# Kernel tuning notes

Measured on AMD Instinct MI355X. Metric: run time of the kernel, lower is better.

## Reference

```python
import jax, jax.numpy as jnp
import numpy as np

N_NODES = 100000
N_EDGES = 3200000
D_IN = 128
D_OUT = 128
LN_EPS = 1e-5


def setup_inputs() -> dict:
    key = jax.random.key(0)
    k1, k2, k3, k4 = jax.random.split(key, 4)
    x = jax.random.normal(k1, (N_NODES, D_IN), dtype=jnp.float32)
    edge_index = jax.random.randint(k2, (2, N_EDGES), 0, N_NODES, dtype=jnp.int64)
    # GCNConv weight (glorot-ish scale) and bias
    W = jax.random.normal(k3, (D_IN, D_OUT), dtype=jnp.float32) / np.sqrt(D_IN)
    b = jnp.zeros((D_OUT,), dtype=jnp.float32)
    # LayerNorm params
    gamma = jnp.ones((D_OUT,), dtype=jnp.float32)
    beta = jnp.zeros((D_OUT,), dtype=jnp.float32)
    return {"x": x, "edge_index": edge_index, "W": W, "b": b, "gamma": gamma, "beta": beta}


def reference(x, edge_index, W, b, gamma, beta):
    # GCNConv: add self-loops, symmetric degree normalization, aggregate, add bias.
    N = x.shape[0]
    self_loops = jnp.arange(N, dtype=edge_index.dtype)
    row = jnp.concatenate([edge_index[0], self_loops])  # destination
    col = jnp.concatenate([edge_index[1], self_loops])  # source
    deg = jax.ops.segment_sum(jnp.ones(row.shape[0], x.dtype), row, num_segments=N)
    dinv = jnp.where(deg > 0, jax.lax.rsqrt(deg), 0.0)
    norm = dinv[row] * dinv[col]                         # [E+N]
    xw = x @ W                                           # [N, D_OUT]
    msg = norm[:, None] * xw[col]                        # gather + scale [E+N, D_OUT]
    agg = jax.ops.segment_sum(msg, row, num_segments=N) + b  # scatter-add
    # LayerNorm over feature dim
    mu = jnp.mean(agg, axis=-1, keepdims=True)
    var = jnp.mean(jnp.square(agg - mu), axis=-1, keepdims=True)
    h = (agg - mu) * jax.lax.rsqrt(var + LN_EPS) * gamma + beta
    # ReLU; Dropout is identity in eval mode
    return jax.nn.relu(h)
```

## Files before the change

### kernel.cpp

```cpp
#include <hip/hip_runtime.h>

#define N_NODES 100000
#define N_EDGES 3200000
#define D 128
#define NB 782
#define BCAP 5120
#define STAGE 16
#define NKEY 1024

typedef __attribute__((ext_vector_type(8))) short bf16x8;
typedef __attribute__((ext_vector_type(4))) float f32x4;

__device__ __forceinline__ float bf2f(unsigned short u) {
  return __uint_as_float(((unsigned)u) << 16);
}
__device__ __forceinline__ unsigned short f2bf(float f) {
  unsigned u = __float_as_uint(f);
  u += 0x7FFF + ((u >> 16) & 1);
  return (unsigned short)(u >> 16);
}

__global__ void detect_kernel(const int* __restrict__ ei32, int* __restrict__ flag) {
  __shared__ int anynz;
  if (threadIdx.x == 0) anynz = 0;
  __syncthreads();
  int v = 0;
  for (int i = threadIdx.x; i < 2048; i += 256) v |= ei32[2 * i + 1];
  if (v) atomicOr(&anynz, 1);
  __syncthreads();
  if (threadIdx.x == 0) *flag = (anynz == 0) ? 1 : 0;
}

__global__ void prep_w_kernel(const float* __restrict__ W, unsigned short* __restrict__ wTg) {
  int t = threadIdx.x;
  int c = t >> 1, h = t & 1;
  for (int k0 = h * 64; k0 < h * 64 + 64; k0 += 8) {
    unsigned short tmp[8];
#pragma unroll
    for (int j = 0; j < 8; j++) tmp[j] = f2bf(W[(k0 + j) * D + c]);
    *(uint4*)(wTg + c * D + k0) = *(uint4*)tmp;
  }
}

__global__ __launch_bounds__(256) void partition_kernel(const void* __restrict__ edges,
                                                        const int* __restrict__ flag,
                                                        int* __restrict__ gcur,
                                                        unsigned int* __restrict__ bstore) {
  __shared__ unsigned int stage[NB][STAGE];
  __shared__ int scnt[NB];
  const bool is64 = (*flag != 0);
  for (int i = threadIdx.x; i < NB; i += 256) scnt[i] = 0;
  __syncthreads();
  int gstride = gridDim.x * blockDim.x;
  for (int base = blockIdx.x * blockDim.x; base < N_EDGES; base += gstride) {
    int e = base + threadIdx.x;
    if (e < N_EDGES) {
      int r, c;
      if (is64) {
        r = (int)((const long long*)edges)[e];
        c = (int)((const long long*)edges)[N_EDGES + e];
      } else {
        r = ((const int*)edges)[e];
        c = ((const int*)edges)[N_EDGES + e];
      }
      int b = r >> 7;
      unsigned ent = ((unsigned)(r & 127) << 17) | (unsigned)c;
      int pos = atomicAdd(&scnt[b], 1);
      if (pos < STAGE) {
        stage[b][pos] = ent;
      } else {
        int gp = atomicAdd(&gcur[b], 1);
        if (gp < BCAP) bstore[(size_t)b * BCAP + gp] = ent;
      }
    }
    __syncthreads();
    for (int b = threadIdx.x; b < NB; b += 256) {
      if (scnt[b] >= STAGE) {
        int gp = atomicAdd(&gcur[b], STAGE);
        if (gp + STAGE <= BCAP) {
          uint4* dst = (uint4*)&bstore[(size_t)b * BCAP + gp];
          uint4* src = (uint4*)&stage[b][0];
          dst[0] = src[0];
          dst[1] = src[1];
          dst[2] = src[2];
          dst[3] = src[3];
        } else {
          for (int k = 0; k < STAGE; k++)
            if (gp + k < BCAP) bstore[(size_t)b * BCAP + gp + k] = stage[b][k];
        }
        scnt[b] = 0;
      }
    }
    __syncthreads();
  }
  for (int b = threadIdx.x; b < NB; b += 256) {
    int n = scnt[b];
    if (n > STAGE) n = STAGE;
    if (n > 0) {
      int gp = atomicAdd(&gcur[b], n);
      for (int k = 0; k < n; k++)
        if (gp + k < BCAP) bstore[(size_t)b * BCAP + gp + k] = stage[b][k];
    }
  }
}

__global__ __launch_bounds__(256) void bucket_kernel(const int* __restrict__ gcur,
                                                     unsigned int* __restrict__ bstore,
                                                     int* __restrict__ cnt,
                                                     int* __restrict__ start,
                                                     float* __restrict__ dinv) {
  __shared__ unsigned int ent[BCAP];
  __shared__ int kc[NKEY];
  __shared__ int koff[NKEY];
  __shared__ int psum[256];
  int b = blockIdx.x, tid = threadIdx.x;
  size_t base = (size_t)b * BCAP;
  int m = gcur[b];
  if (m > BCAP) m = BCAP;
  int nodes = N_NODES - b * 128;
  if (nodes > 128) nodes = 128;

  for (int i = tid; i < m; i += 256) ent[i] = bstore[base + i];
  for (int i = tid; i < NKEY; i += 256) kc[i] = 0;
  __syncthreads();
  for (int i = tid; i < m; i += 256) {
    unsigned u = ent[i];
    int key = (int)(((u >> 17) << 3) | ((u & 0x1FFFFu) >> 14));
    atomicAdd(&kc[key], 1);
  }
  __syncthreads();
  int c0 = kc[4 * tid], c1 = kc[4 * tid + 1], c2 = kc[4 * tid + 2], c3 = kc[4 * tid + 3];
  psum[tid] = c0 + c1 + c2 + c3;
  __syncthreads();
#pragma unroll
  for (int off = 1; off < 256; off <<= 1) {
    int v = (tid >= off) ? psum[tid - off] : 0;
    __syncthreads();
    psum[tid] += v;
    __syncthreads();
  }
  int o = (tid == 0) ? 0 : psum[tid - 1];
  kc[4 * tid] = o;
  kc[4 * tid + 1] = o + c0;
  kc[4 * tid + 2] = o + c0 + c1;
  kc[4 * tid + 3] = o + c0 + c1 + c2;
  koff[4 * tid] = o;
  koff[4 * tid + 1] = o + c0;
  koff[4 * tid + 2] = o + c0 + c1;
  koff[4 * tid + 3] = o + c0 + c1 + c2;
  __syncthreads();
  if (tid < nodes) {
    int st = kc[8 * tid];
    int en = (tid == 127) ? m : kc[8 * (tid + 1)];
    int node = b * 128 + tid;
    start[node] = (int)base + st;
    cnt[node] = en - st;
    dinv[node] = rsqrtf((float)(en - st + 1));
  }
  __syncthreads();
  for (int i = tid; i < m; i += 256) {
    unsigned u = ent[i];
    int key = (int)(((u >> 17) << 3) | ((u & 0x1FFFFu) >> 14));
    int pos = atomicAdd(&koff[key], 1);
    bstore[base + pos] = u & 0x1FFFF;
  }
}

__global__ __launch_bounds__(256) void gemm_mfma_kernel(const float* __restrict__ x,
                                                        const unsigned short* __restrict__ wTg,
                                                        const float* __restrict__ dinv,
                                                        unsigned short* __restrict__ y) {
  __shared__ unsigned short xs[64 * 136];
  __shared__ unsigned short wls[128 * 136];
  int tid = threadIdx.x;
  int row0 = blockIdx.x * 64;
  {
    int c = tid >> 1, h = tid & 1;
    const uint4* src = (const uint4*)(wTg + c * D + h * 64);
    uint4* dst = (uint4*)(wls + c * 136 + h * 64);
#pragma unroll
    for (int i = 0; i < 8; i++) dst[i] = src[i];
  }
  {
    int rx = tid >> 2, q = tid & 3;
    int r = row0 + rx;
    if (r > N_NODES - 1) r = N_NODES - 1;
    const float4* src = (const float4*)(x + (size_t)r * D + q * 32);
    uint4* dst = (uint4*)(xs + rx * 136 + q * 32);
#pragma unroll
    for (int i = 0; i < 4; i++) {
      float4 fa = src[2 * i], fb = src[2 * i + 1];
      uint4 p;
      p.x = (unsigned)f2bf(fa.x) | ((unsigned)f2bf(fa.y) << 16);
      p.y = (unsigned)f2bf(fa.z) | ((unsigned)f2bf(fa.w) << 16);
      p.z = (unsigned)f2bf(fb.x) | ((unsigned)f2bf(fb.y) << 16);
      p.w = (unsigned)f2bf(fb.z) | ((unsigned)f2bf(fb.w) << 16);
      dst[i] = p;
    }
  }
  __syncthreads();
  int w = tid >> 6, l = tid & 63;
  int g = l >> 4, ln = l & 15;
  bf16x8 af[4];
#pragma unroll
  for (int kt = 0; kt < 4; kt++)
    af[kt] = *(const bf16x8*)(xs + (w * 16 + ln) * 136 + kt * 32 + g * 8);
  int rbase = row0 + w * 16 + 4 * g;
  float dv[4];
#pragma unroll
  for (int j = 0; j < 4; j++) {
    int r = rbase + j;
    dv[j] = dinv[r < N_NODES ? r : N_NODES - 1];
  }
#pragma unroll
  for (int ct = 0; ct < 8; ct++) {
    f32x4 acc = {0.f, 0.f, 0.f, 0.f};
#pragma unroll
    for (int kt = 0; kt < 4; kt++) {
      bf16x8 bf = *(const bf16x8*)(wls + (ct * 16 + ln) * 136 + kt * 32 + g * 8);
      acc = __builtin_amdgcn_mfma_f32_16x16x32_bf16(af[kt], bf, acc, 0, 0, 0);
    }
#pragma unroll
    for (int j = 0; j < 4; j++) {
      int r = rbase + j;
      if (r < N_NODES) y[(size_t)r * D + ct * 16 + ln] = f2bf(dv[j] * acc[j]);
    }
  }
}

__global__ __launch_bounds__(256) void agg_ln_kernel(
    const unsigned short* __restrict__ y, const unsigned int* __restrict__ csr,
    const int* __restrict__ start, const int* __restrict__ cnt,
    const float* __restrict__ dinv, const float* __restrict__ bias,
    const float* __restrict__ gamma, const float* __restrict__ beta,
    float* __restrict__ out) {
  int wid = threadIdx.x >> 6, lane = threadIdx.x & 63;
  int node = blockIdx.x * 4 + wid;
  if (node >= N_NODES) return;
  int q = lane >> 4, hl = lane & 15;
  int s = start[node];
  int n = cnt[node];
  float a0 = 0.f, a1 = 0.f, a2 = 0.f, a3 = 0.f, a4 = 0.f, a5 = 0.f, a6 = 0.f, a7 = 0.f;
  const unsigned short* yq = y + hl * 8;
#define ACC(V)                                       \
  a0 += __uint_as_float((V).x << 16);                \
  a1 += __uint_as_float((V).x & 0xFFFF0000u);        \
  a2 += __uint_as_float((V).y << 16);                \
  a3 += __uint_as_float((V).y & 0xFFFF0000u);        \
  a4 += __uint_as_float((V).z << 16);                \
  a5 += __uint_as_float((V).z & 0xFFFF0000u);        \
  a6 += __uint_as_float((V).w << 16);                \
  a7 += __uint_as_float((V).w & 0xFFFF0000u);
  for (int j = 0; j < n; j += 64) {
    int m = n - j;
    if (m > 64) m = 64;
    int cj = (j + lane < n) ? (int)csr[s + j + lane] : 0;
    int t = 0;
    for (; t + 15 < m; t += 16) {
      int e0 = __shfl(cj, t + q);
      int e1 = __shfl(cj, t + 4 + q);
      int e2 = __shfl(cj, t + 8 + q);
      int e3 = __shfl(cj, t + 12 + q);
      uint4 v0 = *(const uint4*)(yq + (size_t)e0 * D);
      uint4 v1 = *(const uint4*)(yq + (size_t)e1 * D);
      uint4 v2 = *(const uint4*)(yq + (size_t)e2 * D);
      uint4 v3 = *(const uint4*)(yq + (size_t)e3 * D);
      ACC(v0) ACC(v1) ACC(v2) ACC(v3)
    }
    for (; t + 3 < m; t += 4) {
      int e0 = __shfl(cj, t + q);
      uint4 v0 = *(const uint4*)(yq + (size_t)e0 * D);
      ACC(v0)
    }
    int rem = m - t;
    if (rem > 0) {
      int sl = t + q;
      if (sl > m - 1) sl = m - 1;
      int e0 = __shfl(cj, sl);
      if (q < rem) {
        uint4 v0 = *(const uint4*)(yq + (size_t)e0 * D);
        ACC(v0)
      }
    }
  }
#define FOLD(A)            \
  A += __shfl_xor(A, 16);  \
  A += __shfl_xor(A, 32);
  FOLD(a0) FOLD(a1) FOLD(a2) FOLD(a3) FOLD(a4) FOLD(a5) FOLD(a6) FOLD(a7)
  uint4 sv = *(const uint4*)(yq + (size_t)node * D);
  ACC(sv)
  float di = dinv[node];
  float4 bi0 = *(const float4*)(bias + hl * 8);
  float4 bi1 = *(const float4*)(bias + hl * 8 + 4);
  float v0 = fmaf(di, a0, bi0.x), v1 = fmaf(di, a1, bi0.y);
  float v2 = fmaf(di, a2, bi0.z), v3 = fmaf(di, a3, bi0.w);
  float v4 = fmaf(di, a4, bi1.x), v5 = fmaf(di, a5, bi1.y);
  float v6 = fmaf(di, a6, bi1.z), v7 = fmaf(di, a7, bi1.w);
  float sum = ((v0 + v1) + (v2 + v3)) + ((v4 + v5) + (v6 + v7));
#pragma unroll
  for (int msk = 1; msk <= 8; msk <<= 1) sum += __shfl_xor(sum, msk);
  float mu = sum * (1.0f / 128.0f);
  float d0 = v0 - mu, d1 = v1 - mu, d2 = v2 - mu, d3 = v3 - mu;
  float d4 = v4 - mu, d5 = v5 - mu, d6 = v6 - mu, d7 = v7 - mu;
  float sq = ((d0 * d0 + d1 * d1) + (d2 * d2 + d3 * d3)) +
             ((d4 * d4 + d5 * d5) + (d6 * d6 + d7 * d7));
#pragma unroll
  for (int msk = 1; msk <= 8; msk <<= 1) sq += __shfl_xor(sq, msk);
  float rstd = rsqrtf(sq * (1.0f / 128.0f) + 1e-5f);
  if (q == 0) {
    float4 ga0 = *(const float4*)(gamma + hl * 8);
    float4 ga1 = *(const float4*)(gamma + hl * 8 + 4);
    float4 be0 = *(const float4*)(beta + hl * 8);
    float4 be1 = *(const float4*)(beta + hl * 8 + 4);
    float4 o0, o1;
    o0.x = fmaxf(fmaf(d0 * rstd, ga0.x, be0.x), 0.0f);
    o0.y = fmaxf(fmaf(d1 * rstd, ga0.y, be0.y), 0.0f);
    o0.z = fmaxf(fmaf(d2 * rstd, ga0.z, be0.z), 0.0f);
    o0.w = fmaxf(fmaf(d3 * rstd, ga0.w, be0.w), 0.0f);
    o1.x = fmaxf(fmaf(d4 * rstd, ga1.x, be1.x), 0.0f);
    o1.y = fmaxf(fmaf(d5 * rstd, ga1.y, be1.y), 0.0f);
    o1.z = fmaxf(fmaf(d6 * rstd, ga1.z, be1.z), 0.0f);
    o1.w = fmaxf(fmaf(d7 * rstd, ga1.w, be1.w), 0.0f);
    *(float4*)(out + (size_t)node * D + hl * 8) = o0;
    *(float4*)(out + (size_t)node * D + hl * 8 + 4) = o1;
  }
#undef ACC
#undef FOLD
}

extern "C" void kernel_launch(void* const* d_in, const int* in_sizes, int n_in,
                              void* d_out, int out_size, void* d_ws, size_t ws_size,
                              hipStream_t stream) {
  const float* x = (const float*)d_in[0];
  const void* edges = d_in[1];
  const float* W = (const float*)d_in[2];
  const float* b = (const float*)d_in[3];
  const float* gamma = (const float*)d_in[4];
  const float* beta = (const float*)d_in[5];
  float* out = (float*)d_out;

  char* w = (char*)d_ws;
  size_t off = 0;
  auto take = [&](size_t bytes) {
    size_t r = off;
    off += (bytes + 255) & ~(size_t)255;
    return r;
  };
  int* flag = (int*)(w + take(256));
  int* gcur = (int*)(w + take((size_t)NB * 4));
  int* cnt = (int*)(w + take((size_t)N_NODES * 4));
  int* start = (int*)(w + take((size_t)N_NODES * 4));
  float* dinv = (float*)(w + take((size_t)N_NODES * 4));
  unsigned short* wTg = (unsigned short*)(w + take((size_t)D * D * 2));
  unsigned int* bstore = (unsigned int*)(w + take((size_t)NB * BCAP * 4));
  unsigned short* y = (unsigned short*)(w + take((size_t)N_NODES * D * 2));

  detect_kernel<<<1, 256, 0, stream>>>((const int*)edges, flag);
  hipMemsetAsync(gcur, 0, (size_t)NB * 4, stream);
  prep_w_kernel<<<1, 256, 0, stream>>>(W, wTg);
  partition_kernel<<<768, 256, 0, stream>>>(edges, flag, gcur, bstore);
  bucket_kernel<<<NB, 256, 0, stream>>>(gcur, bstore, cnt, start, dinv);
  gemm_mfma_kernel<<<(N_NODES + 63) / 64, 256, 0, stream>>>(x, wTg, dinv, y);
  agg_ln_kernel<<<(N_NODES + 3) / 4, 256, 0, stream>>>(y, bstore, start, cnt, dinv, b, gamma,
                                                       beta, out);
}
```

Measured before the change: 328.7 us.

## Fold int64 detection into partition, simplify bucket sort, split aggregation launch

Removes the separate detect kernel by having every partition block sample the edge array to decide whether indices are int64. Parallelizes the W transpose/convert over 16 blocks. The bucket kernel now does a 128-key counting sort by local row instead of a 1024-key sort by row and source sub-range, which drops the source-locality ordering within each row's neighbor list. Aggregation is split into four templated launches of 25000 nodes each, and the bounds check is removed.

```diff
diff --git a/kernel.cpp b/kernel.cpp
--- a/kernel.cpp
+++ b/kernel.cpp
@@ -6,7 +6,7 @@
 #define NB 782
 #define BCAP 5120
 #define STAGE 16
-#define NKEY 1024
+#define QNODES 25000
 
 typedef __attribute__((ext_vector_type(8))) short bf16x8;
 typedef __attribute__((ext_vector_type(4))) float f32x4;
@@ -20,37 +20,33 @@
   return (unsigned short)(u >> 16);
 }
 
-__global__ void detect_kernel(const int* __restrict__ ei32, int* __restrict__ flag) {
-  __shared__ int anynz;
-  if (threadIdx.x == 0) anynz = 0;
-  __syncthreads();
-  int v = 0;
-  for (int i = threadIdx.x; i < 2048; i += 256) v |= ei32[2 * i + 1];
-  if (v) atomicOr(&anynz, 1);
-  __syncthreads();
-  if (threadIdx.x == 0) *flag = (anynz == 0) ? 1 : 0;
-}
-
 __global__ void prep_w_kernel(const float* __restrict__ W, unsigned short* __restrict__ wTg) {
-  int t = threadIdx.x;
-  int c = t >> 1, h = t & 1;
-  for (int k0 = h * 64; k0 < h * 64 + 64; k0 += 8) {
-    unsigned short tmp[8];
-#pragma unroll
-    for (int j = 0; j < 8; j++) tmp[j] = f2bf(W[(k0 + j) * D + c]);
-    *(uint4*)(wTg + c * D + k0) = *(uint4*)tmp;
-  }
+  int idx = blockIdx.x * 256 + threadIdx.x;
+  int c = idx >> 5;
+  int k0 = (idx & 31) * 4;
+  unsigned short tmp[4];
+#pragma unroll
+  for (int j = 0; j < 4; j++) tmp[j] = f2bf(W[(size_t)(k0 + j) * D + c]);
+  *(uint2*)(wTg + (size_t)c * D + k0) = *(uint2*)tmp;
 }
 
 __global__ __launch_bounds__(256) void partition_kernel(const void* __restrict__ edges,
-                                                        const int* __restrict__ flag,
                                                         int* __restrict__ gcur,
                                                         unsigned int* __restrict__ bstore) {
   __shared__ unsigned int stage[NB][STAGE];
   __shared__ int scnt[NB];
-  const bool is64 = (*flag != 0);
+  __shared__ int s_nz;
+  if (threadIdx.x == 0) s_nz = 0;
   for (int i = threadIdx.x; i < NB; i += 256) scnt[i] = 0;
   __syncthreads();
+  {
+    int v = 0;
+    const int* e32 = (const int*)edges;
+    for (int i = threadIdx.x; i < 2048; i += 256) v |= e32[2 * i + 1];
+    if (v) atomicOr(&s_nz, 1);
+  }
+  __syncthreads();
+  const bool is64 = (s_nz == 0);
   int gstride = gridDim.x * blockDim.x;
   for (int base = blockIdx.x * blockDim.x; base < N_EDGES; base += gstride) {
     int e = base + threadIdx.x;
@@ -110,9 +106,9 @@
                                                      int* __restrict__ start,
                                                      float* __restrict__ dinv) {
   __shared__ unsigned int ent[BCAP];
-  __shared__ int kc[NKEY];
-  __shared__ int koff[NKEY];
-  __shared__ int psum[256];
+  __shared__ int lcnt[128];
+  __shared__ int s[128];
+  __shared__ int loffs[128];
   int b = blockIdx.x, tid = threadIdx.x;
   size_t base = (size_t)b * BCAP;
   int m = gcur[b];
@@ -121,47 +117,32 @@
   if (nodes > 128) nodes = 128;
 
   for (int i = tid; i < m; i += 256) ent[i] = bstore[base + i];
-  for (int i = tid; i < NKEY; i += 256) kc[i] = 0;
+  if (tid < 128) lcnt[tid] = 0;
+  __syncthreads();
+  for (int i = tid; i < m; i += 256) atomicAdd(&lcnt[ent[i] >> 17], 1);
+  __syncthreads();
+  if (tid < 128) s[tid] = lcnt[tid];
+  __syncthreads();
+#pragma unroll
+  for (int off = 1; off < 128; off <<= 1) {
+    int v = (tid < 128 && tid >= off) ? s[tid - off] : 0;
+    __syncthreads();
+    if (tid < 128) s[tid] += v;
+    __syncthreads();
+  }
+  if (tid < nodes) {
+    int st = (tid == 0) ? 0 : s[tid - 1];
+    int node = b * 128 + tid;
+    start[node] = (int)base + st;
+    cnt[node] = lcnt[tid];
+    dinv[node] = rsqrtf((float)(lcnt[tid] + 1));
+    loffs[tid] = st;
+  }
   __syncthreads();
   for (int i = tid; i < m; i += 256) {
     unsigned u = ent[i];
-    int key = (int)(((u >> 17) << 3) | ((u & 0x1FFFFu) >> 14));
-    atomicAdd(&kc[key], 1);
-  }
-  __syncthreads();
-  int c0 = kc[4 * tid], c1 = kc[4 * tid + 1], c2 = kc[4 * tid + 2], c3 = kc[4 * tid + 3];
-  psum[tid] = c0 + c1 + c2 + c3;
-  __syncthreads();
-#pragma unroll
-  for (int off = 1; off < 256; off <<= 1) {
-    int v = (tid >= off) ? psum[tid - off] : 0;
-    __syncthreads();
-    psum[tid] += v;
-    __syncthreads();
-  }
-  int o = (tid == 0) ? 0 : psum[tid - 1];
-  kc[4 * tid] = o;
-  kc[4 * tid + 1] = o + c0;
-  kc[4 * tid + 2] = o + c0 + c1;
-  kc[4 * tid + 3] = o + c0 + c1 + c2;
-  koff[4 * tid] = o;
-  koff[4 * tid + 1] = o + c0;
-  koff[4 * tid + 2] = o + c0 + c1;
-  koff[4 * tid + 3] = o + c0 + c1 + c2;
-  __syncthreads();
-  if (tid < nodes) {
-    int st = kc[8 * tid];
-    int en = (tid == 127) ? m : kc[8 * (tid + 1)];
-    int node = b * 128 + tid;
-    start[node] = (int)base + st;
-    cnt[node] = en - st;
-    dinv[node] = rsqrtf((float)(en - st + 1));
-  }
-  __syncthreads();
-  for (int i = tid; i < m; i += 256) {
-    unsigned u = ent[i];
-    int key = (int)(((u >> 17) << 3) | ((u & 0x1FFFFu) >> 14));
-    int pos = atomicAdd(&koff[key], 1);
+    int lr = u >> 17;
+    int pos = atomicAdd(&loffs[lr], 1);
     bstore[base + pos] = u & 0x1FFFF;
   }
 }
@@ -228,6 +209,7 @@
   }
 }
 
+template <int Q>
 __global__ __launch_bounds__(256) void agg_ln_kernel(
     const unsigned short* __restrict__ y, const unsigned int* __restrict__ csr,
     const int* __restrict__ start, const int* __restrict__ cnt,
@@ -235,8 +217,7 @@
     const float* __restrict__ gamma, const float* __restrict__ beta,
     float* __restrict__ out) {
   int wid = threadIdx.x >> 6, lane = threadIdx.x & 63;
-  int node = blockIdx.x * 4 + wid;
-  if (node >= N_NODES) return;
+  int node = Q * QNODES + blockIdx.x * 4 + wid;
   int q = lane >> 4, hl = lane & 15;
   int s = start[node];
   int n = cnt[node];
@@ -346,7 +327,6 @@
     off += (bytes + 255) & ~(size_t)255;
     return r;
   };
-  int* flag = (int*)(w + take(256));
   int* gcur = (int*)(w + take((size_t)NB * 4));
   int* cnt = (int*)(w + take((size_t)N_NODES * 4));
   int* start = (int*)(w + take((size_t)N_NODES * 4));
@@ -355,12 +335,13 @@
   unsigned int* bstore = (unsigned int*)(w + take((size_t)NB * BCAP * 4));
   unsigned short* y = (unsigned short*)(w + take((size_t)N_NODES * D * 2));
 
-  detect_kernel<<<1, 256, 0, stream>>>((const int*)edges, flag);
   hipMemsetAsync(gcur, 0, (size_t)NB * 4, stream);
-  prep_w_kernel<<<1, 256, 0, stream>>>(W, wTg);
-  partition_kernel<<<768, 256, 0, stream>>>(edges, flag, gcur, bstore);
+  prep_w_kernel<<<16, 256, 0, stream>>>(W, wTg);
+  partition_kernel<<<768, 256, 0, stream>>>(edges, gcur, bstore);
   bucket_kernel<<<NB, 256, 0, stream>>>(gcur, bstore, cnt, start, dinv);
   gemm_mfma_kernel<<<(N_NODES + 63) / 64, 256, 0, stream>>>(x, wTg, dinv, y);
-  agg_ln_kernel<<<(N_NODES + 3) / 4, 256, 0, stream>>>(y, bstore, start, cnt, dinv, b, gamma,
-                                                       beta, out);
-}
+  agg_ln_kernel<0><<<QNODES / 4, 256, 0, stream>>>(y, bstore, start, cnt, dinv, b, gamma, beta, out);
+  agg_ln_kernel<1><<<QNODES / 4, 256, 0, stream>>>(y, bstore, start, cnt, dinv, b, gamma, beta, out);
+  agg_ln_kernel<2><<<QNODES / 4, 256, 0, stream>>>(y, bstore, start, cnt, dinv, b, gamma, beta, out);
+  agg_ln_kernel<3><<<QNODES / 4, 256, 0, stream>>>(y, bstore, start, cnt, dinv, b, gamma, beta, out);
+}
```

Measured after the change: 336.4 us. +2.3%, slower.
